# Optimization experiments

Hardware: AMD Instinct MI355X
Metric: run time of the kernel (lower is better)

## Reference

```python
import jax, jax.numpy as jnp
import numpy as np

SIGMA = 2.0

def _gaussian_kernel_2d(sigma, dtype=jnp.float32):
    # neurite utils.gaussian_kernel: windowsize = round(3*sigma)*2 + 1 per dim,
    # separable gaussian, full ND kernel normalized to sum to 1.
    ws = int(round(3.0 * sigma) * 2 + 1)  # 13 for sigma=2
    mid = (ws - 1) / 2.0
    x = jnp.arange(ws, dtype=dtype) - mid
    g = jnp.exp(-(x * x) / (2.0 * sigma * sigma))  # unnormalized 1D gaussian
    k = jnp.outer(g, g)                            # [ws, ws]
    return k / jnp.sum(k)


def setup_inputs() -> dict:
    key = jax.random.key(0)
    x = jax.random.normal(key, (32, 384, 384, 16), dtype=jnp.float32)
    return {"x": x}


def reference(x) -> jnp.ndarray:
    # Original: per-channel tf.nn.conv2d with the same [ws,ws,1,1] gaussian
    # kernel, SAME padding, then concat. Equivalent single depthwise conv:
    C = x.shape[-1]
    k = _gaussian_kernel_2d(SIGMA, x.dtype)                 # [ws, ws]
    kern = jnp.tile(k[:, :, None, None], (1, 1, 1, C))      # HWIO, groups=C
    return jax.lax.conv_general_dilated(
        x, kern,
        window_strides=(1, 1),
        padding='SAME',
        dimension_numbers=('NHWC', 'HWIO', 'NHWC'),
        feature_group_count=C,
    )
```

## Files before the change

### kernel.cpp

```cpp
#include <hip/hip_runtime.h>
#include <cmath>

#define GH 384
#define GW 384
#define GN 32
#define C4 4
#define RAD 6
#define KS 13
#define TW 32
#define TH 16
#define LROWS (TH + 2*RAD)
#define PXH 8
#define PYV 8

struct Wt13 { float w[KS]; };

__global__ __launch_bounds__(256)
void gauss13_kernel(const float4* __restrict__ x, float4* __restrict__ y, Wt13 wt) {
    __shared__ float4 lds[LROWS][TW][C4];

    const int tid = threadIdx.x;
    const int w0 = blockIdx.x * TW;
    const int h0 = blockIdx.y * TH;
    const int n  = blockIdx.z;

    {
        const int c4    = tid & 3;
        const int colg  = (tid >> 2) & 3;
        const int lrow0 = tid >> 4;
        #pragma unroll
        for (int it = 0; it < 2; ++it) {
            const int lrow = lrow0 + it * 16;
            if (lrow < LROWS) {
                const int gr = h0 - RAD + lrow;
                float4 ld[PXH + 2*RAD];
                if (gr >= 0 && gr < GH) {
                    const float4* rowp = x + (size_t)(n * GH + gr) * GW * C4 + c4;
                    #pragma unroll
                    for (int k = 0; k < PXH + 2*RAD; ++k) {
                        const int gw = w0 + colg * PXH - RAD + k;
                        ld[k] = (gw >= 0 && gw < GW) ? rowp[(size_t)gw * C4]
                                                     : make_float4(0.f, 0.f, 0.f, 0.f);
                    }
                } else {
                    #pragma unroll
                    for (int k = 0; k < PXH + 2*RAD; ++k)
                        ld[k] = make_float4(0.f, 0.f, 0.f, 0.f);
                }
                #pragma unroll
                for (int p = 0; p < PXH; ++p) {
                    float sx = 0.f, sy = 0.f, sz = 0.f, sw = 0.f;
                    #pragma unroll
                    for (int k = 0; k < KS; ++k) {
                        const float g = wt.w[k];
                        sx += ld[p + k].x * g;
                        sy += ld[p + k].y * g;
                        sz += ld[p + k].z * g;
                        sw += ld[p + k].w * g;
                    }
                    lds[lrow][colg * PXH + p][c4] = make_float4(sx, sy, sz, sw);
                }
            }
        }
    }
    __syncthreads();

    {
        const int c4  = tid & 3;
        const int col = (tid >> 2) & 31;
        const int r0  = (tid >> 7) * PYV;
        float4 acc[PYV];
        #pragma unroll
        for (int i = 0; i < PYV; ++i) acc[i] = make_float4(0.f, 0.f, 0.f, 0.f);
        #pragma unroll
        for (int t = 0; t < PYV + 2*RAD; ++t) {
            const float4 v = lds[r0 + t][col][c4];
            #pragma unroll
            for (int i = 0; i < PYV; ++i) {
                const int k = t - i;
                if (k >= 0 && k < KS) {
                    const float g = wt.w[k];
                    acc[i].x += v.x * g;
                    acc[i].y += v.y * g;
                    acc[i].z += v.z * g;
                    acc[i].w += v.w * g;
                }
            }
        }
        float4* outp = y + ((size_t)(n * GH + h0 + r0) * GW + (w0 + col)) * C4 + c4;
        #pragma unroll
        for (int i = 0; i < PYV; ++i)
            outp[(size_t)i * GW * C4] = acc[i];
    }
}

extern "C" void kernel_launch(void* const* d_in, const int* in_sizes, int n_in,
                              void* d_out, int out_size, void* d_ws, size_t ws_size,
                              hipStream_t stream) {
    const float4* x = (const float4*)d_in[0];
    float4* y = (float4*)d_out;

    Wt13 wt;
    double g[KS], s = 0.0;
    for (int i = 0; i < KS; ++i) { double d = i - 6.0; g[i] = exp(-(d * d) / 8.0); s += g[i]; }
    for (int i = 0; i < KS; ++i) wt.w[i] = (float)(g[i] / s);

    dim3 grid(GW / TW, GH / TH, GN);
    gauss13_kernel<<<grid, 256, 0, stream>>>(x, y, wt);
}
```

Baseline: 518.7 us.

## Use 512-thread blocks, XCD-aware block remap, swizzled LDS, nontemporal stores

The block size doubles to 512 threads. Each thread now handles one horizontal-pass row and four vertical outputs instead of eight, which raises parallelism per tile and lowers register pressure. Block indices are remapped so that neighbouring tiles land on the same XCD, improving L2 reuse of halo rows. LDS addresses get an XOR swizzle on odd rows to reduce bank conflicts, and output stores are nontemporal to avoid polluting the cache. The risks are more vertical-pass overhead per output and possible occupancy limits from the larger blocks.

```diff
diff --git a/kernel.cpp b/kernel.cpp
--- a/kernel.cpp
+++ b/kernel.cpp
@@ -11,55 +11,68 @@
 #define TH 16
 #define LROWS (TH + 2*RAD)
 #define PXH 8
-#define PYV 8
+#define PYV 4
+#define NTHREADS 512
 
 struct Wt13 { float w[KS]; };
 
-__global__ __launch_bounds__(256)
+typedef float v4f __attribute__((ext_vector_type(4)));
+
+__device__ __forceinline__ int lidx(int r, int col, int c4) {
+    int i = (r * TW + col) * C4 + c4;
+    return i ^ ((r & 1) << 2);
+}
+
+__global__ __launch_bounds__(NTHREADS, 4)
 void gauss13_kernel(const float4* __restrict__ x, float4* __restrict__ y, Wt13 wt) {
-    __shared__ float4 lds[LROWS][TW][C4];
+    __shared__ float4 lds4[LROWS * TW * C4];
+
+    const int nwgx = GW / TW;
+    const int nwgy = GH / TH;
+    const int lin  = blockIdx.x + nwgx * (blockIdx.y + nwgy * blockIdx.z);
+    const int per  = (nwgx * nwgy * GN) >> 3;
+    const int swz  = (lin & 7) * per + (lin >> 3);
+    const int bx   = swz % nwgx;
+    const int by   = (swz / nwgx) % nwgy;
+    const int bz   = swz / (nwgx * nwgy);
 
     const int tid = threadIdx.x;
-    const int w0 = blockIdx.x * TW;
-    const int h0 = blockIdx.y * TH;
-    const int n  = blockIdx.z;
+    const int w0 = bx * TW;
+    const int h0 = by * TH;
+    const int n  = bz;
 
     {
-        const int c4    = tid & 3;
-        const int colg  = (tid >> 2) & 3;
-        const int lrow0 = tid >> 4;
-        #pragma unroll
-        for (int it = 0; it < 2; ++it) {
-            const int lrow = lrow0 + it * 16;
-            if (lrow < LROWS) {
-                const int gr = h0 - RAD + lrow;
-                float4 ld[PXH + 2*RAD];
-                if (gr >= 0 && gr < GH) {
-                    const float4* rowp = x + (size_t)(n * GH + gr) * GW * C4 + c4;
-                    #pragma unroll
-                    for (int k = 0; k < PXH + 2*RAD; ++k) {
-                        const int gw = w0 + colg * PXH - RAD + k;
-                        ld[k] = (gw >= 0 && gw < GW) ? rowp[(size_t)gw * C4]
-                                                     : make_float4(0.f, 0.f, 0.f, 0.f);
-                    }
-                } else {
-                    #pragma unroll
-                    for (int k = 0; k < PXH + 2*RAD; ++k)
-                        ld[k] = make_float4(0.f, 0.f, 0.f, 0.f);
+        const int c4   = tid & 3;
+        const int colg = (tid >> 2) & 3;
+        const int lrow = tid >> 4;
+        if (lrow < LROWS) {
+            const int gr = h0 - RAD + lrow;
+            float4 ld[PXH + 2*RAD];
+            if (gr >= 0 && gr < GH) {
+                const float4* rowp = x + (size_t)(n * GH + gr) * GW * C4 + c4;
+                #pragma unroll
+                for (int k = 0; k < PXH + 2*RAD; ++k) {
+                    const int gw = w0 + colg * PXH - RAD + k;
+                    ld[k] = (gw >= 0 && gw < GW) ? rowp[(size_t)gw * C4]
+                                                 : make_float4(0.f, 0.f, 0.f, 0.f);
                 }
+            } else {
                 #pragma unroll
-                for (int p = 0; p < PXH; ++p) {
-                    float sx = 0.f, sy = 0.f, sz = 0.f, sw = 0.f;
-                    #pragma unroll
-                    for (int k = 0; k < KS; ++k) {
-                        const float g = wt.w[k];
-                        sx += ld[p + k].x * g;
-                        sy += ld[p + k].y * g;
-                        sz += ld[p + k].z * g;
-                        sw += ld[p + k].w * g;
-                    }
-                    lds[lrow][colg * PXH + p][c4] = make_float4(sx, sy, sz, sw);
+                for (int k = 0; k < PXH + 2*RAD; ++k)
+                    ld[k] = make_float4(0.f, 0.f, 0.f, 0.f);
+            }
+            #pragma unroll
+            for (int p = 0; p < PXH; ++p) {
+                float sx = 0.f, sy = 0.f, sz = 0.f, sw = 0.f;
+                #pragma unroll
+                for (int k = 0; k < KS; ++k) {
+                    const float g = wt.w[k];
+                    sx += ld[p + k].x * g;
+                    sy += ld[p + k].y * g;
+                    sz += ld[p + k].z * g;
+                    sw += ld[p + k].w * g;
                 }
+                lds4[lidx(lrow, colg * PXH + p, c4)] = make_float4(sx, sy, sz, sw);
             }
         }
     }
@@ -74,7 +87,7 @@
         for (int i = 0; i < PYV; ++i) acc[i] = make_float4(0.f, 0.f, 0.f, 0.f);
         #pragma unroll
         for (int t = 0; t < PYV + 2*RAD; ++t) {
-            const float4 v = lds[r0 + t][col][c4];
+            const float4 v = lds4[lidx(r0 + t, col, c4)];
             #pragma unroll
             for (int i = 0; i < PYV; ++i) {
                 const int k = t - i;
@@ -89,8 +102,10 @@
         }
         float4* outp = y + ((size_t)(n * GH + h0 + r0) * GW + (w0 + col)) * C4 + c4;
         #pragma unroll
-        for (int i = 0; i < PYV; ++i)
-            outp[(size_t)i * GW * C4] = acc[i];
+        for (int i = 0; i < PYV; ++i) {
+            v4f v; v.x = acc[i].x; v.y = acc[i].y; v.z = acc[i].z; v.w = acc[i].w;
+            __builtin_nontemporal_store(v, reinterpret_cast<v4f*>(outp + (size_t)i * GW * C4));
+        }
     }
 }
 
@@ -106,5 +121,5 @@
     for (int i = 0; i < KS; ++i) wt.w[i] = (float)(g[i] / s);
 
     dim3 grid(GW / TW, GH / TH, GN);
-    gauss13_kernel<<<grid, 256, 0, stream>>>(x, y, wt);
+    gauss13_kernel<<<grid, NTHREADS, 0, stream>>>(x, y, wt);
 }
```

Result: no change. 515.3 us (-0.7%).
